# Optimization experiments

Hardware: AMD Instinct MI355X
Metric: run time of the kernel (lower is better)

## Reference

```python
import jax, jax.numpy as jnp
import numpy as np

N_NODES = 100000
N_EDGES = 1600000
IN_FEATS = 128
H_FEATS = 64
NEG_SLOPE = 0.2


def gat_layer(x, W, a_l, a_r, b, src, dst):
    # x: [N, Fin], W: [Fin, Fout], a_l/a_r/b: [Fout]
    h = x @ W                                   # [N, Fout]
    el = h @ a_l                                # [N]
    er = h @ a_r                                # [N]
    e = el[src] + er[dst]                       # [E]
    e = jnp.where(e > 0, e, NEG_SLOPE * e)      # leaky_relu
    # segment softmax over incoming edges of each dst node
    m = jax.ops.segment_max(e, dst, num_segments=N_NODES)   # [N], -inf for deg-0
    ex = jnp.exp(e - m[dst])                                 # [E]
    s = jax.ops.segment_sum(ex, dst, num_segments=N_NODES)   # [N]
    alpha = ex / s[dst]                                      # [E]
    out = jax.ops.segment_sum(alpha[:, None] * h[src], dst, num_segments=N_NODES)
    return jax.nn.relu(out + b)


def setup_inputs() -> dict:
    key = jax.random.key(0)
    ks = jax.random.split(key, 16)
    in_feat = jax.random.normal(ks[0], (N_NODES, IN_FEATS), dtype=jnp.float32)
    src = jax.random.randint(ks[1], (N_EDGES,), 0, N_NODES, dtype=jnp.int32)
    dst = jax.random.randint(ks[2], (N_EDGES,), 0, N_NODES, dtype=jnp.int32)
    def w(k, fin, fout):
        return jax.random.normal(k, (fin, fout), dtype=jnp.float32) * (1.0 / np.sqrt(fin))
    def v(k, f):
        return jax.random.normal(k, (f,), dtype=jnp.float32) * 0.1
    return {
        "in_feat": in_feat, "src": src, "dst": dst,
        "W1": w(ks[3], IN_FEATS, H_FEATS), "al1": v(ks[4], H_FEATS), "ar1": v(ks[5], H_FEATS), "b1": jnp.zeros((H_FEATS,), jnp.float32),
        "W2": w(ks[6], H_FEATS, H_FEATS), "al2": v(ks[7], H_FEATS), "ar2": v(ks[8], H_FEATS), "b2": jnp.zeros((H_FEATS,), jnp.float32),
        "W3": w(ks[9], H_FEATS, H_FEATS), "al3": v(ks[10], H_FEATS), "ar3": v(ks[11], H_FEATS), "b3": jnp.zeros((H_FEATS,), jnp.float32),
    }


def reference(in_feat, src, dst, W1, al1, ar1, b1, W2, al2, ar2, b2, W3, al3, ar3, b3):
    h = gat_layer(in_feat, W1, al1, ar1, b1, src, dst)
    h = gat_layer(h, W2, al2, ar2, b2, src, dst)
    h = gat_layer(h, W3, al3, ar3, b3, src, dst)
    return h
```

## Files before the change

### kernel.cpp

```cpp
#include <hip/hip_runtime.h>
#include <hip/hip_fp16.h>
#include <math.h>

#define HF 64
#define LEAKY 0.2f
#define NBLK 256
#define NPB 512
#define MAXNB 256
#define STAGE_CAP 9216

typedef _Float16 half4_t __attribute__((ext_vector_type(4)));
typedef _Float16 half8_t __attribute__((ext_vector_type(8)));
typedef float floatx4 __attribute__((ext_vector_type(4)));


__global__ __launch_bounds__(256)
void part_count(const int* __restrict__ dst, int* __restrict__ Cmat, int E, int nb) {
    __shared__ int lc[MAXNB];
    int tid = threadIdx.x;
    for (int t = tid; t < nb; t += 256) lc[t] = 0;
    __syncthreads();
    int chunk = (E + NBLK - 1) / NBLK;
    int b0 = blockIdx.x * chunk, b1 = min(b0 + chunk, E);
    for (int i = b0 + tid; i < b1; i += 256)
        atomicAdd(&lc[dst[i] >> 9], 1);
    __syncthreads();
    for (int t = tid; t < nb; t += 256) Cmat[t * NBLK + blockIdx.x] = lc[t];
}

__global__ __launch_bounds__(256)
void scan_offsets(const int* __restrict__ Cmat, int* __restrict__ Omat,
                  int* __restrict__ bbase, int E, int nb) {
    __shared__ int tot[256];
    int t = threadIdx.x;
    int s = 0;
    if (t < nb)
        for (int blk = 0; blk < NBLK; ++blk) s += Cmat[t * NBLK + blk];
    tot[t] = s;
    __syncthreads();
    for (int off = 1; off < 256; off <<= 1) {
        int u = (t >= off) ? tot[t - off] : 0;
        __syncthreads();
        tot[t] += u;
        __syncthreads();
    }
    int excl = tot[t] - s;
    if (t < nb) {
        bbase[t] = excl;
        int run = excl;
        for (int blk = 0; blk < NBLK; ++blk) {
            Omat[t * NBLK + blk] = run;
            run += Cmat[t * NBLK + blk];
        }
    }
    if (t == 0) bbase[nb] = E;
}

__global__ __launch_bounds__(256)
void part_scatter(const int* __restrict__ src, const int* __restrict__ dst,
                  const int* __restrict__ Omat, int* __restrict__ part, int E, int nb) {
    __shared__ int ocur[MAXNB];
    int tid = threadIdx.x;
    for (int t = tid; t < nb; t += 256) ocur[t] = Omat[t * NBLK + blockIdx.x];
    __syncthreads();
    int chunk = (E + NBLK - 1) / NBLK;
    int b0 = blockIdx.x * chunk, b1 = min(b0 + chunk, E);
    for (int i = b0 + tid; i < b1; i += 256) {
        int s = src[i], d = dst[i];
        int pos = atomicAdd(&ocur[d >> 9], 1);
        part[pos] = ((d & (NPB - 1)) << 17) | s;
    }
}

__global__ __launch_bounds__(NPB)
void bucket_csr(const int* __restrict__ part, const int* __restrict__ bbase,
                int* __restrict__ row_ptr, int* __restrict__ ssrc, int N, int E, int nb) {
    int b = blockIdx.x, tid = threadIdx.x;
    int bstart = bbase[b], bend = bbase[b + 1];
    int len = bend - bstart;
    int nb0 = b << 9;
    __shared__ int cnt[NPB];
    __shared__ int stage[STAGE_CAP];
    cnt[tid] = 0;
    bool staged = (len <= STAGE_CAP);
    __syncthreads();
    if (staged) {
        for (int i = tid; i < len; i += NPB) {
            int v = part[bstart + i];
            stage[i] = v;
            atomicAdd(&cnt[v >> 17], 1);
        }
    } else {
        for (int i = tid; i < len; i += NPB)
            atomicAdd(&cnt[part[bstart + i] >> 17], 1);
    }
    __syncthreads();
    int v = cnt[tid];
    for (int off = 1; off < NPB; off <<= 1) {
        int u = (tid >= off) ? cnt[tid - off] : 0;
        __syncthreads();
        cnt[tid] += u;
        __syncthreads();
    }
    int excl = cnt[tid] - v;
    int node = nb0 + tid;
    if (node < N) row_ptr[node] = bstart + excl;
    __syncthreads();
    cnt[tid] = bstart + excl;
    __syncthreads();
    if (staged) {
        for (int i = tid; i < len; i += NPB) {
            int e = stage[i];
            int slot = atomicAdd(&cnt[e >> 17], 1);
            ssrc[slot] = e & 0x1FFFF;
        }
    } else {
        for (int i = tid; i < len; i += NPB) {
            int e = part[bstart + i];
            int slot = atomicAdd(&cnt[e >> 17], 1);
            ssrc[slot] = e & 0x1FFFF;
        }
    }
    if (b == nb - 1 && tid == 0) row_ptr[N] = E;
}


template <int K, bool XF16>
__global__ __launch_bounds__(256, 3)
void gemm_mfma(const void* __restrict__ Xv, const float* __restrict__ W,
               const float* __restrict__ al, const float* __restrict__ ar,
               __half* __restrict__ H2, float* __restrict__ el, float* __restrict__ er,
               int n, int nslabs) {
    constexpr int KS = K / 32;
    int lane = threadIdx.x & 63;
    int li = lane & 15, g = lane >> 4;
    int wid = blockIdx.x * 4 + (threadIdx.x >> 6);
    int wstride = gridDim.x * 4;

    half8_t bf[4][KS];
    float alv[4], arv[4];
#pragma unroll
    for (int ct = 0; ct < 4; ++ct) {
        int col = ct * 16 + li;
        alv[ct] = al[col];
        arv[ct] = ar[col];
#pragma unroll
        for (int ks = 0; ks < KS; ++ks) {
            half8_t b;
#pragma unroll
            for (int j = 0; j < 4; ++j) {
                b[j]     = (_Float16)W[(ks * 32 + 4 * g + j) * 64 + col];
                b[4 + j] = (_Float16)W[(ks * 32 + 16 + 4 * g + j) * 64 + col];
            }
            bf[ct][ks] = b;
        }
    }

    for (int s = wid; s < nslabs; s += wstride) {
        int row = s * 16 + li;
        int rc = row < n ? row : n - 1;

        half8_t a[KS];
#pragma unroll
        for (int ks = 0; ks < KS; ++ks) {
            if constexpr (XF16) {
                const __half* Xh = (const __half*)Xv;
                half4_t h0 = *(const half4_t*)(Xh + (size_t)rc * K + ks * 32 + 4 * g);
                half4_t h1 = *(const half4_t*)(Xh + (size_t)rc * K + ks * 32 + 16 + 4 * g);
                half8_t av;
#pragma unroll
                for (int j = 0; j < 4; ++j) { av[j] = h0[j]; av[4 + j] = h1[j]; }
                a[ks] = av;
            } else {
                const float* Xf = (const float*)Xv;
                float4 v0 = *(const float4*)(Xf + (size_t)rc * K + ks * 32 + 4 * g);
                float4 v1 = *(const float4*)(Xf + (size_t)rc * K + ks * 32 + 16 + 4 * g);
                half8_t av;
                av[0] = (_Float16)v0.x; av[1] = (_Float16)v0.y;
                av[2] = (_Float16)v0.z; av[3] = (_Float16)v0.w;
                av[4] = (_Float16)v1.x; av[5] = (_Float16)v1.y;
                av[6] = (_Float16)v1.z; av[7] = (_Float16)v1.w;
                a[ks] = av;
            }
        }

        floatx4 acc[4];
#pragma unroll
        for (int ct = 0; ct < 4; ++ct) acc[ct] = (floatx4){0.f, 0.f, 0.f, 0.f};
#pragma unroll
        for (int ks = 0; ks < KS; ++ks)
#pragma unroll
            for (int ct = 0; ct < 4; ++ct)
                acc[ct] = __builtin_amdgcn_mfma_f32_16x16x32_f16(a[ks], bf[ct][ks], acc[ct], 0, 0, 0);

        float pl[4], pr[4];
#pragma unroll
        for (int r = 0; r < 4; ++r) {
            pl[r] = acc[0][r] * alv[0] + acc[1][r] * alv[1] + acc[2][r] * alv[2] + acc[3][r] * alv[3];
            pr[r] = acc[0][r] * arv[0] + acc[1][r] * arv[1] + acc[2][r] * arv[2] + acc[3][r] * arv[3];
        }
#pragma unroll
        for (int r = 0; r < 4; ++r)
#pragma unroll
            for (int off = 1; off < 16; off <<= 1) {
                pl[r] += __shfl_xor(pl[r], off);
                pr[r] += __shfl_xor(pr[r], off);
            }
        int rowbase = s * 16 + 4 * g;
#pragma unroll
        for (int r = 0; r < 4; ++r) {
            int ro = rowbase + r;
            if (ro < n) {
#pragma unroll
                for (int ct = 0; ct < 4; ++ct)
                    H2[(size_t)ro * HF + ct * 16 + li] = __float2half(acc[ct][r]);
                if (li == 0) { el[ro] = pl[r]; er[ro] = pr[r]; }
            }
        }
    }
}


template <bool YF16>
__device__ __forceinline__
void node_fullwave(int node, const int* __restrict__ row_ptr, const int* __restrict__ ssrc,
                   const float* __restrict__ el, const float* __restrict__ er,
                   const uint2* __restrict__ H2v, const __half* __restrict__ H2,
                   float4 bv, const float* __restrict__ b, void* __restrict__ Y,
                   int lane, int g, int fl) {
    int s0 = row_ptr[node], s1 = row_ptr[node + 1];
    int d = s1 - s0;
    float ern = er[node];

    if (d <= 64) {
        int sidx = 0;
        float e = -INFINITY;
        if (lane < d) {
            sidx = ssrc[s0 + lane];
            e = el[sidx] + ern;
            e = e > 0.f ? e : LEAKY * e;
        }
        float p = (lane < d) ? __expf(e) : 0.f;

        float4 acc = make_float4(0.f, 0.f, 0.f, 0.f);
        int nchunk = (d + 31) >> 5;
        for (int c = 0; c < nchunk; ++c) {
            int jb = c * 32 + g;
            int ss[8];
            float pp[8];
#pragma unroll
            for (int u = 0; u < 8; ++u) {
                ss[u] = __shfl(sidx, jb + 4 * u);
                pp[u] = __shfl(p, jb + 4 * u);
            }
            uint2 vv[8];
#pragma unroll
            for (int u = 0; u < 8; ++u) vv[u] = H2v[(size_t)ss[u] * 16 + fl];
#pragma unroll
            for (int u = 0; u < 8; ++u) {
                __half2 a = *(__half2*)&vv[u].x;
                __half2 b2 = *(__half2*)&vv[u].y;
                float2 fa = __half22float2(a);
                float2 fb = __half22float2(b2);
                acc.x = fmaf(pp[u], fa.x, acc.x);
                acc.y = fmaf(pp[u], fa.y, acc.y);
                acc.z = fmaf(pp[u], fb.x, acc.z);
                acc.w = fmaf(pp[u], fb.y, acc.w);
            }
        }
        float psum = p;
#pragma unroll
        for (int off = 32; off; off >>= 1) psum += __shfl_xor(psum, off);
#pragma unroll
        for (int off = 16; off <= 32; off <<= 1) {
            acc.x += __shfl_xor(acc.x, off);
            acc.y += __shfl_xor(acc.y, off);
            acc.z += __shfl_xor(acc.z, off);
            acc.w += __shfl_xor(acc.w, off);
        }
        float inv = d ? 1.f / psum : 0.f;
        float4 o;
        o.x = fmaf(acc.x, inv, bv.x);
        o.y = fmaf(acc.y, inv, bv.y);
        o.z = fmaf(acc.z, inv, bv.z);
        o.w = fmaf(acc.w, inv, bv.w);
        o.x = o.x > 0.f ? o.x : 0.f;
        o.y = o.y > 0.f ? o.y : 0.f;
        o.z = o.z > 0.f ? o.z : 0.f;
        o.w = o.w > 0.f ? o.w : 0.f;
        if (g == 0) {
            if constexpr (YF16) {
                __half2 a = __floats2half2_rn(o.x, o.y);
                __half2 c = __floats2half2_rn(o.z, o.w);
                ((uint2*)Y)[(size_t)node * 16 + fl] = make_uint2(*(unsigned*)&a, *(unsigned*)&c);
            } else {
                ((float4*)Y)[(size_t)node * 16 + fl] = o;
            }
        }
    } else {
        float acc = 0.f, psum = 0.f;
        for (int j = s0; j < s1; ++j) {
            int s = ssrc[j];
            float e = el[s] + ern;
            e = e > 0.f ? e : LEAKY * e;
            float p = __expf(e);
            psum += p;
            acc = fmaf(p, __half2float(H2[(size_t)s * HF + lane]), acc);
        }
        float o = acc / psum + b[lane];
        o = o > 0.f ? o : 0.f;
        if constexpr (YF16)
            ((__half*)Y)[(size_t)node * HF + lane] = __float2half(o);
        else
            ((float*)Y)[(size_t)node * HF + lane] = o;
    }
}

template <bool YF16>
__global__ __launch_bounds__(256)
void edge_kernel(const int* __restrict__ row_ptr, const int* __restrict__ ssrc,
                 const float* __restrict__ el, const float* __restrict__ er,
                 const __half* __restrict__ H2, const float* __restrict__ b,
                 void* __restrict__ Y, int n) {
    int lane = threadIdx.x & 63;
    int half = lane >> 5, hl = lane & 31;
    int g = lane >> 4, fl = lane & 15;
    const uint2* H2v = (const uint2*)H2;
    float4 bv = ((const float4*)b)[fl];
    int npairs = (n + 1) >> 1;
    int wid = blockIdx.x * 4 + (threadIdx.x >> 6);
    int nwaves = gridDim.x * 4;
    int PP = (npairs + nwaves - 1) / nwaves;
    int p0 = wid * PP;
    int p1 = min(p0 + PP, npairs);
    if (p0 >= p1) return;
    int cntp = p1 - p0;

    int rp = 0;
    if (lane <= 2 * cntp) rp = row_ptr[min(2 * p0 + lane, n)];

    auto fetch = [&](int i, int& dd, int& sidx, float& elv, float& ernv) {
        int myNode = 2 * (p0 + i) + half;
        bool ok = myNode < n;
        int s0 = __shfl(rp, 2 * i + half);
        int s1 = __shfl(rp, 2 * i + half + 1);
        dd = ok ? (s1 - s0) : 0;
        sidx = 0; elv = -INFINITY; ernv = 0.f;
        if (ok) ernv = er[myNode];
        if (hl < dd && dd <= 32) {
            sidx = ssrc[s0 + hl];
            elv = el[sidx];
        }
    };

    int d_c, s_c; float el_c, er_c;
    fetch(0, d_c, s_c, el_c, er_c);

    for (int i = 0; i < cntp; ++i) {
        int dA = __shfl(d_c, 0), dB = __shfl(d_c, 32);
        bool hasnext = (i + 1 < cntp);
        int d_n = 0, s_n = 0; float el_n = 0.f, er_n = 0.f;
        int myNode = 2 * (p0 + i) + half;
        bool ok = myNode < n;

        if (dA <= 32 && dB <= 32) {
            float e = el_c + er_c;
            e = e > 0.f ? e : LEAKY * e;
            float p = (hl < d_c) ? __expf(e) : 0.f;

            if (hasnext) fetch(i + 1, d_n, s_n, el_n, er_n);

            float4 acc = make_float4(0.f, 0.f, 0.f, 0.f);
            int dg = (g >> 1) ? dB : dA;
            int hbase = (g >> 1) << 5;
            int gpar = g & 1;
            int nch = (dg + 15) >> 4;
            for (int c = 0; c < nch; ++c) {
                int ss[8];
                float pp[8];
#pragma unroll
                for (int u = 0; u < 8; ++u) {
                    int sl = hbase + c * 16 + 2 * u + gpar;
                    ss[u] = __shfl(s_c, sl);
                    pp[u] = __shfl(p, sl);
                }
                uint2 vv[8];
#pragma unroll
                for (int u = 0; u < 8; ++u) vv[u] = H2v[(size_t)ss[u] * 16 + fl];
#pragma unroll
                for (int u = 0; u < 8; ++u) {
                    __half2 a = *(__half2*)&vv[u].x;
                    __half2 b2 = *(__half2*)&vv[u].y;
                    float2 fa = __half22float2(a);
                    float2 fb = __half22float2(b2);
                    acc.x = fmaf(pp[u], fa.x, acc.x);
                    acc.y = fmaf(pp[u], fa.y, acc.y);
                    acc.z = fmaf(pp[u], fb.x, acc.z);
                    acc.w = fmaf(pp[u], fb.y, acc.w);
                }
            }
            float psum = p;
#pragma unroll
            for (int off = 16; off; off >>= 1) psum += __shfl_xor(psum, off);
            acc.x += __shfl_xor(acc.x, 16);
            acc.y += __shfl_xor(acc.y, 16);
            acc.z += __shfl_xor(acc.z, 16);
            acc.w += __shfl_xor(acc.w, 16);
            float inv = d_c ? 1.f / psum : 0.f;
            float4 o;
            o.x = fmaf(acc.x, inv, bv.x);
            o.y = fmaf(acc.y, inv, bv.y);
            o.z = fmaf(acc.z, inv, bv.z);
            o.w = fmaf(acc.w, inv, bv.w);
            o.x = o.x > 0.f ? o.x : 0.f;
            o.y = o.y > 0.f ? o.y : 0.f;
            o.z = o.z > 0.f ? o.z : 0.f;
            o.w = o.w > 0.f ? o.w : 0.f;
            if (!(g & 1) && ok) {
                if constexpr (YF16) {
                    __half2 a = __floats2half2_rn(o.x, o.y);
                    __half2 c2 = __floats2half2_rn(o.z, o.w);
                    ((uint2*)Y)[(size_t)myNode * 16 + fl] = make_uint2(*(unsigned*)&a, *(unsigned*)&c2);
                } else {
                    ((float4*)Y)[(size_t)myNode * 16 + fl] = o;
                }
            }
        } else {
            if (hasnext) fetch(i + 1, d_n, s_n, el_n, er_n);
            int nodeA = 2 * (p0 + i);
            node_fullwave<YF16>(nodeA, row_ptr, ssrc, el, er, H2v, H2, bv, b, Y, lane, g, fl);
            if (nodeA + 1 < n)
                node_fullwave<YF16>(nodeA + 1, row_ptr, ssrc, el, er, H2v, H2, bv, b, Y, lane, g, fl);
        }

        d_c = d_n; s_c = s_n; el_c = el_n; er_c = er_n;
    }
}


extern "C" void kernel_launch(void* const* d_in, const int* in_sizes, int n_in,
                              void* d_out, int out_size, void* d_ws, size_t ws_size,
                              hipStream_t stream) {
    const int N = in_sizes[0] / 128;
    const int E = in_sizes[1];
    const int nb = (N + NPB - 1) >> 9;

    const float* in_feat = (const float*)d_in[0];
    const int* src = (const int*)d_in[1];
    const int* dst = (const int*)d_in[2];
    const float* W1 = (const float*)d_in[3];
    const float* al1 = (const float*)d_in[4];
    const float* ar1 = (const float*)d_in[5];
    const float* b1 = (const float*)d_in[6];
    const float* W2 = (const float*)d_in[7];
    const float* al2 = (const float*)d_in[8];
    const float* ar2 = (const float*)d_in[9];
    const float* b2 = (const float*)d_in[10];
    const float* W3 = (const float*)d_in[11];
    const float* al3 = (const float*)d_in[12];
    const float* ar3 = (const float*)d_in[13];
    const float* b3 = (const float*)d_in[14];

    char* ws = (char*)d_ws;
    size_t off = 0;
    auto alloc = [&](size_t bytes) {
        void* p = ws + off;
        off += (bytes + 255) & ~(size_t)255;
        return p;
    };
    int* row_ptr = (int*)alloc(((size_t)N + 1) * 4);
    int* ssrc = (int*)alloc((size_t)E * 4);
    int* part = (int*)alloc((size_t)E * 4);
    int* Cmat = (int*)alloc((size_t)MAXNB * NBLK * 4);
    int* Omat = (int*)alloc((size_t)MAXNB * NBLK * 4);
    int* bbase = (int*)alloc(((size_t)MAXNB + 1) * 4);
    float* el = (float*)alloc((size_t)N * 4);
    float* er = (float*)alloc((size_t)N * 4);
    __half* H2buf = (__half*)alloc((size_t)N * HF * 2);
    __half* Y2buf = (__half*)alloc((size_t)N * HF * 2);

    part_count<<<NBLK, 256, 0, stream>>>(dst, Cmat, E, nb);
    scan_offsets<<<1, 256, 0, stream>>>(Cmat, Omat, bbase, E, nb);
    part_scatter<<<NBLK, 256, 0, stream>>>(src, dst, Omat, part, E, nb);
    bucket_csr<<<nb, NPB, 0, stream>>>(part, bbase, row_ptr, ssrc, N, E, nb);

    int nslabs = (N + 15) / 16;
    int gg = 512;
    int ge = 2048;

    gemm_mfma<128, false><<<gg, 256, 0, stream>>>(in_feat, W1, al1, ar1, H2buf, el, er, N, nslabs);
    edge_kernel<true><<<ge, 256, 0, stream>>>(row_ptr, ssrc, el, er, H2buf, b1, Y2buf, N);
    gemm_mfma<64, true><<<gg, 256, 0, stream>>>(Y2buf, W2, al2, ar2, H2buf, el, er, N, nslabs);
    edge_kernel<true><<<ge, 256, 0, stream>>>(row_ptr, ssrc, el, er, H2buf, b2, Y2buf, N);
    gemm_mfma<64, true><<<gg, 256, 0, stream>>>(Y2buf, W3, al3, ar3, H2buf, el, er, N, nslabs);
    edge_kernel<false><<<ge, 256, 0, stream>>>(row_ptr, ssrc, el, er, H2buf, b3, d_out, N);
}
```

Before: 230.4 us.

## Shrink CSR buckets, stage W in LDS, prefetch GEMM rows, reorder edge shuffles

Buckets for CSR construction drop from 512 to 256 nodes. This doubles the bucket count, which raises bucket_csr parallelism and lowers its shared-memory footprint, but makes the single-block scan larger. The GEMM now copies W into shared memory before building its fragments and software-pipelines the next slab's A loads behind the current MFMAs; it also drops the occupancy hint. The edge kernel issues the gather loads before the probability shuffles so memory latency can overlap.

```diff
diff --git a/kernel.cpp b/kernel.cpp
--- a/kernel.cpp
+++ b/kernel.cpp
@@ -5,9 +5,9 @@
 #define HF 64
 #define LEAKY 0.2f
 #define NBLK 256
-#define NPB 512
-#define MAXNB 256
-#define STAGE_CAP 9216
+#define NPB 256
+#define MAXNB 512
+#define STAGE_CAP 5120
 
 typedef _Float16 half4_t __attribute__((ext_vector_type(4)));
 typedef _Float16 half8_t __attribute__((ext_vector_type(8)));
@@ -23,22 +23,22 @@
     int chunk = (E + NBLK - 1) / NBLK;
     int b0 = blockIdx.x * chunk, b1 = min(b0 + chunk, E);
     for (int i = b0 + tid; i < b1; i += 256)
-        atomicAdd(&lc[dst[i] >> 9], 1);
+        atomicAdd(&lc[dst[i] >> 8], 1);
     __syncthreads();
     for (int t = tid; t < nb; t += 256) Cmat[t * NBLK + blockIdx.x] = lc[t];
 }
 
-__global__ __launch_bounds__(256)
+__global__ __launch_bounds__(512)
 void scan_offsets(const int* __restrict__ Cmat, int* __restrict__ Omat,
                   int* __restrict__ bbase, int E, int nb) {
-    __shared__ int tot[256];
+    __shared__ int tot[512];
     int t = threadIdx.x;
     int s = 0;
     if (t < nb)
         for (int blk = 0; blk < NBLK; ++blk) s += Cmat[t * NBLK + blk];
     tot[t] = s;
     __syncthreads();
-    for (int off = 1; off < 256; off <<= 1) {
+    for (int off = 1; off < 512; off <<= 1) {
         int u = (t >= off) ? tot[t - off] : 0;
         __syncthreads();
         tot[t] += u;
@@ -67,7 +67,7 @@
     int b0 = blockIdx.x * chunk, b1 = min(b0 + chunk, E);
     for (int i = b0 + tid; i < b1; i += 256) {
         int s = src[i], d = dst[i];
-        int pos = atomicAdd(&ocur[d >> 9], 1);
+        int pos = atomicAdd(&ocur[d >> 8], 1);
         part[pos] = ((d & (NPB - 1)) << 17) | s;
     }
 }
@@ -78,7 +78,7 @@
     int b = blockIdx.x, tid = threadIdx.x;
     int bstart = bbase[b], bend = bbase[b + 1];
     int len = bend - bstart;
-    int nb0 = b << 9;
+    int nb0 = b << 8;
     __shared__ int cnt[NPB];
     __shared__ int stage[STAGE_CAP];
     cnt[tid] = 0;
@@ -126,12 +126,18 @@
 
 
 template <int K, bool XF16>
-__global__ __launch_bounds__(256, 3)
+__global__ __launch_bounds__(256)
 void gemm_mfma(const void* __restrict__ Xv, const float* __restrict__ W,
                const float* __restrict__ al, const float* __restrict__ ar,
                __half* __restrict__ H2, float* __restrict__ el, float* __restrict__ er,
                int n, int nslabs) {
     constexpr int KS = K / 32;
+    __shared__ float Wl[K * 64];
+    int tid = threadIdx.x;
+    for (int i = tid; i < K * 16; i += 256)
+        ((float4*)Wl)[i] = ((const float4*)W)[i];
+    __syncthreads();
+
     int lane = threadIdx.x & 63;
     int li = lane & 15, g = lane >> 4;
     int wid = blockIdx.x * 4 + (threadIdx.x >> 6);
@@ -149,18 +155,16 @@
             half8_t b;
 #pragma unroll
             for (int j = 0; j < 4; ++j) {
-                b[j]     = (_Float16)W[(ks * 32 + 4 * g + j) * 64 + col];
-                b[4 + j] = (_Float16)W[(ks * 32 + 16 + 4 * g + j) * 64 + col];
+                b[j]     = (_Float16)Wl[(ks * 32 + 4 * g + j) * 64 + col];
+                b[4 + j] = (_Float16)Wl[(ks * 32 + 16 + 4 * g + j) * 64 + col];
             }
             bf[ct][ks] = b;
         }
     }
 
-    for (int s = wid; s < nslabs; s += wstride) {
+    auto loadA = [&](int s, half8_t (&a)[KS]) {
         int row = s * 16 + li;
         int rc = row < n ? row : n - 1;
-
-        half8_t a[KS];
 #pragma unroll
         for (int ks = 0; ks < KS; ++ks) {
             if constexpr (XF16) {
@@ -183,6 +187,17 @@
                 a[ks] = av;
             }
         }
+    };
+
+    int s0 = wid;
+    if (s0 >= nslabs) return;
+    half8_t a_c[KS];
+    loadA(s0, a_c);
+
+    for (int s = s0; s < nslabs; s += wstride) {
+        int snext = s + wstride;
+        half8_t a_n[KS];
+        if (snext < nslabs) loadA(snext, a_n);
 
         floatx4 acc[4];
 #pragma unroll
@@ -191,7 +206,7 @@
         for (int ks = 0; ks < KS; ++ks)
 #pragma unroll
             for (int ct = 0; ct < 4; ++ct)
-                acc[ct] = __builtin_amdgcn_mfma_f32_16x16x32_f16(a[ks], bf[ct][ks], acc[ct], 0, 0, 0);
+                acc[ct] = __builtin_amdgcn_mfma_f32_16x16x32_f16(a_c[ks], bf[ct][ks], acc[ct], 0, 0, 0);
 
         float pl[4], pr[4];
 #pragma unroll
@@ -216,6 +231,11 @@
                     H2[(size_t)ro * HF + ct * 16 + li] = __float2half(acc[ct][r]);
                 if (li == 0) { el[ro] = pl[r]; er[ro] = pr[r]; }
             }
+        }
+
+        if (snext < nslabs) {
+#pragma unroll
+            for (int ks = 0; ks < KS; ++ks) a_c[ks] = a_n[ks];
         }
     }
 }
@@ -377,16 +397,16 @@
             int nch = (dg + 15) >> 4;
             for (int c = 0; c < nch; ++c) {
                 int ss[8];
+#pragma unroll
+                for (int u = 0; u < 8; ++u)
+                    ss[u] = __shfl(s_c, hbase + c * 16 + 2 * u + gpar);
+                uint2 vv[8];
+#pragma unroll
+                for (int u = 0; u < 8; ++u) vv[u] = H2v[(size_t)ss[u] * 16 + fl];
                 float pp[8];
 #pragma unroll
-                for (int u = 0; u < 8; ++u) {
-                    int sl = hbase + c * 16 + 2 * u + gpar;
-                    ss[u] = __shfl(s_c, sl);
-                    pp[u] = __shfl(p, sl);
-                }
-                uint2 vv[8];
-#pragma unroll
-                for (int u = 0; u < 8; ++u) vv[u] = H2v[(size_t)ss[u] * 16 + fl];
+                for (int u = 0; u < 8; ++u)
+                    pp[u] = __shfl(p, hbase + c * 16 + 2 * u + gpar);
 #pragma unroll
                 for (int u = 0; u < 8; ++u) {
                     __half2 a = *(__half2*)&vv[u].x;
@@ -443,7 +463,7 @@
                               hipStream_t stream) {
     const int N = in_sizes[0] / 128;
     const int E = in_sizes[1];
-    const int nb = (N + NPB - 1) >> 9;
+    const int nb = (N + NPB - 1) >> 8;
 
     const float* in_feat = (const float*)d_in[0];
     const int* src = (const int*)d_in[1];
@@ -480,7 +500,7 @@
     __half* Y2buf = (__half*)alloc((size_t)N * HF * 2);
 
     part_count<<<NBLK, 256, 0, stream>>>(dst, Cmat, E, nb);
-    scan_offsets<<<1, 256, 0, stream>>>(Cmat, Omat, bbase, E, nb);
+    scan_offsets<<<1, 512, 0, stream>>>(Cmat, Omat, bbase, E, nb);
     part_scatter<<<NBLK, 256, 0, stream>>>(src, dst, Omat, part, E, nb);
     bucket_csr<<<nb, NPB, 0, stream>>>(part, bbase, row_ptr, ssrc, N, E, nb);
 
```

New measurement: 254.1 us. 1.1x slower.
